# Performance work log

Measured on AMD Instinct MI355X. Metric: run time of the kernel, lower is better.

The kernel has to match this reference:

```python
import jax, jax.numpy as jnp
import numpy as np

TOKEN_NUMS = 206
IGNORE_IDX = -100
HALF_TOKEN = float((TOKEN_NUMS - 4) / 2)  # 101.0

B, S = 256, 682
T = 3 * S + 2  # 2048


def setup_inputs() -> dict:
    key = jax.random.key(0)
    k1, k2, k3, k4 = jax.random.split(key, 4)
    pred = jax.random.normal(k1, (B, T, TOKEN_NUMS), dtype=jnp.float32)
    gt_acc = jax.random.uniform(k2, (B, S), dtype=jnp.float32)
    gt_steer = jax.random.uniform(k3, (B, S), dtype=jnp.float32)
    gt_reverse = jax.random.randint(k4, (B, S), 0, 2, dtype=jnp.int64)
    return {"pred": pred, "gt_acc": gt_acc, "gt_steer": gt_steer, "gt_reverse": gt_reverse}


def _smooth_l1(pred, target):
    d = pred - target
    ad = jnp.abs(d)
    return jnp.mean(jnp.where(ad < 1.0, 0.5 * d * d, ad - 0.5))


def reference(pred, gt_acc, gt_steer, gt_reverse):
    pred_control = pred[:, :-2, :]
    acc_logits = pred_control[:, 0::3, :]    # [B, S, V]
    steer_logits = pred_control[:, 1::3, :]  # [B, S, V]
    rev_logits = pred_control[:, 2::3, :]    # [B, S, V]

    # softmax followed by argmax == argmax of logits (softmax is monotonic)
    acc_idx = jnp.argmax(acc_logits, axis=-1).reshape(-1).astype(jnp.float32)
    # vectorized detokenize_acc: if token > half: t/half - 1 else -(t/half - 1)
    pred_acc = jnp.where(acc_idx > HALF_TOKEN, acc_idx / HALF_TOKEN - 1.0,
                         1.0 - acc_idx / HALF_TOKEN)
    acc_val_loss = _smooth_l1(pred_acc, gt_acc.reshape(-1))

    steer_idx = jnp.argmax(steer_logits, axis=-1).reshape(-1).astype(jnp.float32)
    pred_steer = steer_idx / HALF_TOKEN - 1.0  # detokenize_steer
    steer_val_loss = _smooth_l1(pred_steer, gt_steer.reshape(-1))

    acc_steer_val_loss = acc_val_loss + steer_val_loss

    # reverse branch: sum softmax prob mass over the two token ranges per row
    rev_probs = jax.nn.softmax(rev_logits.reshape(-1, TOKEN_NUMS), axis=-1)
    p_no_reverse = jnp.sum(rev_probs[:, :101], axis=-1)
    p_reverse = jnp.sum(rev_probs[:, 101:], axis=-1)
    two_class = jnp.stack([p_no_reverse, p_reverse], axis=-1)  # [N, 2]
    # nn.CrossEntropyLoss applies log_softmax to its input (here: probabilities)
    logp = jax.nn.log_softmax(two_class, axis=-1)
    gt = gt_reverse.reshape(-1)
    valid = gt != IGNORE_IDX
    gt_safe = jnp.where(valid, gt, 0)
    nll = -jnp.take_along_axis(logp, gt_safe[:, None], axis=1)[:, 0]
    reverse_val_loss = jnp.sum(jnp.where(valid, nll, 0.0)) / jnp.maximum(
        jnp.sum(valid.astype(jnp.float32)), 1.0)

    return acc_steer_val_loss, reverse_val_loss
```

## Files before the change

kernel.cpp:

```cpp
#include <hip/hip_runtime.h>
#include <cstddef>

namespace {
constexpr int TOK   = 206;
constexpr int NROWS = 256 * 682;
constexpr int R     = 8;
constexpr int NBLK  = NROWS / R;
constexpr int LROW2 = 310;
constexpr int LDSF2 = R * LROW2 + 16;
constexpr int NSLOT = 64;
}

typedef float f32x4 __attribute__((ext_vector_type(4)));

__global__ __launch_bounds__(256) void cvl_main(
    const float* __restrict__ pred,
    const float* __restrict__ gt_acc,
    const float* __restrict__ gt_steer,
    const int*  __restrict__ gt_rev,
    double* __restrict__ ws)
{
    __shared__ alignas(16) double lds2[LDSF2];

    const int tid = threadIdx.x;
    const int r0  = blockIdx.x * R;

    const int sr = tid >> 5;
    const int sc = tid & 31;
    const int row = r0 + sr;
    const unsigned bb = (unsigned)row / 682u;
    const float* base = pred + (size_t)(3u * (unsigned)row + 2u * bb) * TOK;

    f32x4 v[5];
    #pragma unroll
    for (int k = 0; k < 4; ++k)
        v[k] = __builtin_nontemporal_load((const f32x4*)base + sc + 32 * k);
    const bool t5 = (sc < 26);
    f32x4 v4 = (f32x4){0.f, 0.f, 0.f, 0.f};
    if (t5) v4 = __builtin_nontemporal_load((const f32x4*)base + sc + 128);
    double tl = 0.0;
    if (sc == 31)
        tl = __builtin_nontemporal_load((const double*)(base + 616));
    const int   gt = gt_rev[row];
    const float ga = gt_acc[row];
    const float gs = gt_steer[row];

    f32x4* lrow4 = (f32x4*)(lds2 + sr * LROW2);
    #pragma unroll
    for (int k = 0; k < 4; ++k) lrow4[sc + 32 * k] = v[k];
    if (t5) lrow4[sc + 128] = v4;
    if (sc == 31) lds2[sr * LROW2 + 308] = tl;
    __syncthreads();

    const int lane = tid & 63;
    const int wid  = tid >> 6;
    const int l32  = lane & 31;
    const double* rp = &lds2[sr * LROW2];

    float2 q[10];
    #pragma unroll
    for (int k = 0; k < 10; ++k)
        q[k] = __builtin_bit_cast(float2, rp[l32 + 32 * k]);

    float aM = q[0].x; int aI = 2 * l32;
    if (q[0].y > aM) { aM = q[0].y; aI = 2 * l32 + 1; }
    #pragma unroll
    for (int k = 1; k <= 2; ++k) {
        const int t = 2 * (l32 + 32 * k);
        if (q[k].x > aM) { aM = q[k].x; aI = t; }
        if (q[k].y > aM) { aM = q[k].y; aI = t + 1; }
    }
    float sM = -INFINITY; int sI = 0;
    {
        const int i2 = l32 + 96;
        if (l32 < 7) {
            if (q[3].x > aM) { aM = q[3].x; aI = 2 * i2; }
            if (q[3].y > aM) { aM = q[3].y; aI = 2 * i2 + 1; }
        } else {
            sM = q[3].x; sI = 2 * i2 - 206;
            if (q[3].y > sM) { sM = q[3].y; sI = 2 * i2 - 205; }
        }
    }
    #pragma unroll
    for (int k = 4; k <= 5; ++k) {
        const int st = 2 * (l32 + 32 * k) - 206;
        if (q[k].x > sM) { sM = q[k].x; sI = st; }
        if (q[k].y > sM) { sM = q[k].y; sI = st + 1; }
    }
    float lo = 0.f, hi = 0.f;
    {
        if (l32 < 14) {
            const int st = 2 * (l32 + 192) - 206;
            if (q[6].x > sM) { sM = q[6].x; sI = st; }
            if (q[6].y > sM) { sM = q[6].y; sI = st + 1; }
        } else {
            lo += __expf(q[6].x) + __expf(q[6].y);
        }
    }
    lo += __expf(q[7].x) + __expf(q[7].y);
    {
        const float ex = __expf(q[8].x), ey = __expf(q[8].y);
        if (l32 == 0) lo += ex; else hi += ex;
        hi += ey;
    }
    if (l32 < 21) hi += __expf(q[9].x) + __expf(q[9].y);

    #pragma unroll
    for (int off = 16; off >= 1; off >>= 1) {
        const float av = __shfl_xor(aM, off);
        const int   ai = __shfl_xor(aI, off);
        if (av > aM) { aM = av; aI = ai; }
        const float sv = __shfl_xor(sM, off);
        const int   si = __shfl_xor(sI, off);
        if (sv > sM) { sM = sv; sI = si; }
        lo += __shfl_xor(lo, off);
        hi += __shfl_xor(hi, off);
    }

    float accS, steerS, revS = 0.f, cntS = 0.f;
    {
        const float Z    = lo + hi;
        const float pno  = lo / Z;
        const float prv  = hi / Z;
        const float ai_f = (float)aI;
        const float si_f = (float)sI;
        const float pa   = (ai_f > 101.f) ? (ai_f * (1.f / 101.f) - 1.f)
                                          : (1.f - ai_f * (1.f / 101.f));
        const float ps   = si_f * (1.f / 101.f) - 1.f;
        const float da   = pa - ga;
        const float dsv  = ps - gs;
        const float ada  = fabsf(da), ads = fabsf(dsv);
        accS   = (ada < 1.f) ? 0.5f * da * da   : ada - 0.5f;
        steerS = (ads < 1.f) ? 0.5f * dsv * dsv : ads - 0.5f;
        if (gt != -100) {
            const float m2 = fmaxf(pno, prv);
            revS = m2 + __logf(__expf(pno - m2) + __expf(prv - m2))
                   - ((gt == 0) ? pno : prv);
            cntS = 1.f;
        }
    }

    accS   += __shfl_xor(accS, 32);
    steerS += __shfl_xor(steerS, 32);
    revS   += __shfl_xor(revS, 32);
    cntS   += __shfl_xor(cntS, 32);

    __shared__ float red[4][4];
    if (lane == 0) {
        red[wid][0] = accS; red[wid][1] = steerS;
        red[wid][2] = revS; red[wid][3] = cntS;
    }
    __syncthreads();
    if (tid == 0) {
        double a = 0, st = 0, rr = 0, c = 0;
        for (int w = 0; w < 4; ++w) {
            a += red[w][0]; st += red[w][1]; rr += red[w][2]; c += red[w][3];
        }
        double* slot = ws + (size_t)(blockIdx.x & (NSLOT - 1)) * 4;
        atomicAdd(slot + 0, a);
        atomicAdd(slot + 1, st);
        atomicAdd(slot + 2, rr);
        atomicAdd(slot + 3, c);
    }
}

__global__ void cvl_init(double* __restrict__ ws) {
    const int i = blockIdx.x * blockDim.x + threadIdx.x;
    if (i < NSLOT * 4) ws[i] = 0.0;
}

__global__ void cvl_final(const double* __restrict__ ws, float* __restrict__ out) {
    const int t = threadIdx.x;
    double a = ws[4 * t], st = ws[4 * t + 1], r = ws[4 * t + 2], c = ws[4 * t + 3];
    #pragma unroll
    for (int off = 32; off >= 1; off >>= 1) {
        a  += __shfl_xor(a,  off);
        st += __shfl_xor(st, off);
        r  += __shfl_xor(r,  off);
        c  += __shfl_xor(c,  off);
    }
    if (t == 0) {
        const double n = (double)NROWS;
        out[0] = (float)(a / n + st / n);
        out[1] = (float)(r / fmax(c, 1.0));
    }
}

extern "C" void kernel_launch(void* const* d_in, const int* in_sizes, int n_in,
                              void* d_out, int out_size, void* d_ws, size_t ws_size,
                              hipStream_t stream) {
    const float* pred     = (const float*)d_in[0];
    const float* gt_acc   = (const float*)d_in[1];
    const float* gt_steer = (const float*)d_in[2];
    const int*   gt_rev   = (const int*)d_in[3];
    double* ws  = (double*)d_ws;
    float*  out = (float*)d_out;

    cvl_init<<<1, 256, 0, stream>>>(ws);
    cvl_main<<<NBLK, 256, 0, stream>>>(pred, gt_acc, gt_steer, gt_rev, ws);
    cvl_final<<<1, 64, 0, stream>>>(ws, out);
}
```

Baseline: 86.79 us.

## Use persistent grid-stride blocks with register prefetch of the next row group

The kernel moves from one block per 8-row group (21824 blocks) to a fixed grid of 2048 persistent blocks that loop over groups. Each block issues the global loads for its next group into registers right after the LDS barrier, so they overlap with the current group's argmax and softmax work. Partial sums now accumulate across iterations, which cuts the number of per-block atomics. The cost is higher register pressure from keeping the prefetch buffers live, which may lower occupancy and reduce the memory parallelism this bandwidth-bound kernel depends on.

```diff
diff --git a/kernel.cpp b/kernel.cpp
--- a/kernel.cpp
+++ b/kernel.cpp
@@ -5,7 +5,8 @@
 constexpr int TOK   = 206;
 constexpr int NROWS = 256 * 682;
 constexpr int R     = 8;
-constexpr int NBLK  = NROWS / R;
+constexpr int NGRP  = NROWS / R;
+constexpr int GRID  = 2048;
 constexpr int LROW2 = 310;
 constexpr int LDSF2 = R * LROW2 + 16;
 constexpr int NSLOT = 64;
@@ -23,121 +24,134 @@
     __shared__ alignas(16) double lds2[LDSF2];
 
     const int tid = threadIdx.x;
-    const int r0  = blockIdx.x * R;
-
-    const int sr = tid >> 5;
-    const int sc = tid & 31;
-    const int row = r0 + sr;
-    const unsigned bb = (unsigned)row / 682u;
-    const float* base = pred + (size_t)(3u * (unsigned)row + 2u * bb) * TOK;
-
-    f32x4 v[5];
-    #pragma unroll
-    for (int k = 0; k < 4; ++k)
-        v[k] = __builtin_nontemporal_load((const f32x4*)base + sc + 32 * k);
-    const bool t5 = (sc < 26);
-    f32x4 v4 = (f32x4){0.f, 0.f, 0.f, 0.f};
-    if (t5) v4 = __builtin_nontemporal_load((const f32x4*)base + sc + 128);
-    double tl = 0.0;
-    if (sc == 31)
-        tl = __builtin_nontemporal_load((const double*)(base + 616));
-    const int   gt = gt_rev[row];
-    const float ga = gt_acc[row];
-    const float gs = gt_steer[row];
-
-    f32x4* lrow4 = (f32x4*)(lds2 + sr * LROW2);
-    #pragma unroll
-    for (int k = 0; k < 4; ++k) lrow4[sc + 32 * k] = v[k];
-    if (t5) lrow4[sc + 128] = v4;
-    if (sc == 31) lds2[sr * LROW2 + 308] = tl;
-    __syncthreads();
-
+    const int sr  = tid >> 5;
+    const int sc  = tid & 31;
     const int lane = tid & 63;
     const int wid  = tid >> 6;
     const int l32  = lane & 31;
-    const double* rp = &lds2[sr * LROW2];
-
-    float2 q[10];
-    #pragma unroll
-    for (int k = 0; k < 10; ++k)
-        q[k] = __builtin_bit_cast(float2, rp[l32 + 32 * k]);
-
-    float aM = q[0].x; int aI = 2 * l32;
-    if (q[0].y > aM) { aM = q[0].y; aI = 2 * l32 + 1; }
-    #pragma unroll
-    for (int k = 1; k <= 2; ++k) {
-        const int t = 2 * (l32 + 32 * k);
-        if (q[k].x > aM) { aM = q[k].x; aI = t; }
-        if (q[k].y > aM) { aM = q[k].y; aI = t + 1; }
-    }
-    float sM = -INFINITY; int sI = 0;
-    {
-        const int i2 = l32 + 96;
-        if (l32 < 7) {
-            if (q[3].x > aM) { aM = q[3].x; aI = 2 * i2; }
-            if (q[3].y > aM) { aM = q[3].y; aI = 2 * i2 + 1; }
-        } else {
-            sM = q[3].x; sI = 2 * i2 - 206;
-            if (q[3].y > sM) { sM = q[3].y; sI = 2 * i2 - 205; }
-        }
-    }
-    #pragma unroll
-    for (int k = 4; k <= 5; ++k) {
-        const int st = 2 * (l32 + 32 * k) - 206;
-        if (q[k].x > sM) { sM = q[k].x; sI = st; }
-        if (q[k].y > sM) { sM = q[k].y; sI = st + 1; }
-    }
-    float lo = 0.f, hi = 0.f;
-    {
-        if (l32 < 14) {
-            const int st = 2 * (l32 + 192) - 206;
-            if (q[6].x > sM) { sM = q[6].x; sI = st; }
-            if (q[6].y > sM) { sM = q[6].y; sI = st + 1; }
-        } else {
-            lo += __expf(q[6].x) + __expf(q[6].y);
-        }
-    }
-    lo += __expf(q[7].x) + __expf(q[7].y);
-    {
-        const float ex = __expf(q[8].x), ey = __expf(q[8].y);
-        if (l32 == 0) lo += ex; else hi += ex;
-        hi += ey;
-    }
-    if (l32 < 21) hi += __expf(q[9].x) + __expf(q[9].y);
-
-    #pragma unroll
-    for (int off = 16; off >= 1; off >>= 1) {
-        const float av = __shfl_xor(aM, off);
-        const int   ai = __shfl_xor(aI, off);
-        if (av > aM) { aM = av; aI = ai; }
-        const float sv = __shfl_xor(sM, off);
-        const int   si = __shfl_xor(sI, off);
-        if (sv > sM) { sM = sv; sI = si; }
-        lo += __shfl_xor(lo, off);
-        hi += __shfl_xor(hi, off);
-    }
-
-    float accS, steerS, revS = 0.f, cntS = 0.f;
-    {
-        const float Z    = lo + hi;
-        const float pno  = lo / Z;
-        const float prv  = hi / Z;
-        const float ai_f = (float)aI;
-        const float si_f = (float)sI;
-        const float pa   = (ai_f > 101.f) ? (ai_f * (1.f / 101.f) - 1.f)
-                                          : (1.f - ai_f * (1.f / 101.f));
-        const float ps   = si_f * (1.f / 101.f) - 1.f;
-        const float da   = pa - ga;
-        const float dsv  = ps - gs;
-        const float ada  = fabsf(da), ads = fabsf(dsv);
-        accS   = (ada < 1.f) ? 0.5f * da * da   : ada - 0.5f;
-        steerS = (ads < 1.f) ? 0.5f * dsv * dsv : ads - 0.5f;
-        if (gt != -100) {
-            const float m2 = fmaxf(pno, prv);
-            revS = m2 + __logf(__expf(pno - m2) + __expf(prv - m2))
-                   - ((gt == 0) ? pno : prv);
-            cntS = 1.f;
-        }
+
+    float accS = 0.f, steerS = 0.f, revS = 0.f, cntS = 0.f;
+
+    f32x4 v[5];
+    double tl = 0.0;
+    int   gtN; float gaN, gsN;
+    auto load_group = [&](int g) {
+        const int row = g * R + sr;
+        const unsigned bb = (unsigned)row / 682u;
+        const float* base = pred + (size_t)(3u * (unsigned)row + 2u * bb) * TOK;
+        #pragma unroll
+        for (int k = 0; k < 4; ++k)
+            v[k] = __builtin_nontemporal_load((const f32x4*)base + sc + 32 * k);
+        if (sc < 26)
+            v[4] = __builtin_nontemporal_load((const f32x4*)base + sc + 128);
+        if (sc == 31)
+            tl = __builtin_nontemporal_load((const double*)(base + 616));
+        gtN = gt_rev[row];
+        gaN = gt_acc[row];
+        gsN = gt_steer[row];
+    };
+
+    int g = blockIdx.x;
+    if (g < NGRP) load_group(g);
+
+    while (g < NGRP) {
+        f32x4* lrow4 = (f32x4*)(lds2 + sr * LROW2);
+        #pragma unroll
+        for (int k = 0; k < 4; ++k) lrow4[sc + 32 * k] = v[k];
+        if (sc < 26) lrow4[sc + 128] = v[4];
+        if (sc == 31) lds2[sr * LROW2 + 308] = tl;
+        const int   gt = gtN;
+        const float ga = gaN;
+        const float gs = gsN;
+        __syncthreads();
+
+        const int gn = g + GRID;
+        if (gn < NGRP) load_group(gn);
+
+        const double* rp = &lds2[sr * LROW2];
+        float2 q[10];
+        #pragma unroll
+        for (int k = 0; k < 10; ++k)
+            q[k] = __builtin_bit_cast(float2, rp[l32 + 32 * k]);
+
+        float aM = q[0].x; int aI = 2 * l32;
+        if (q[0].y > aM) { aM = q[0].y; aI = 2 * l32 + 1; }
+        #pragma unroll
+        for (int k = 1; k <= 2; ++k) {
+            const int t = 2 * (l32 + 32 * k);
+            if (q[k].x > aM) { aM = q[k].x; aI = t; }
+            if (q[k].y > aM) { aM = q[k].y; aI = t + 1; }
+        }
+        float sM = -INFINITY; int sI = 0;
+        {
+            const int i2 = l32 + 96;
+            if (l32 < 7) {
+                if (q[3].x > aM) { aM = q[3].x; aI = 2 * i2; }
+                if (q[3].y > aM) { aM = q[3].y; aI = 2 * i2 + 1; }
+            } else {
+                sM = q[3].x; sI = 2 * i2 - 206;
+                if (q[3].y > sM) { sM = q[3].y; sI = 2 * i2 - 205; }
+            }
+        }
+        #pragma unroll
+        for (int k = 4; k <= 5; ++k) {
+            const int st = 2 * (l32 + 32 * k) - 206;
+            if (q[k].x > sM) { sM = q[k].x; sI = st; }
+            if (q[k].y > sM) { sM = q[k].y; sI = st + 1; }
+        }
+        float lo = 0.f, hi = 0.f;
+        {
+            if (l32 < 14) {
+                const int st = 2 * (l32 + 192) - 206;
+                if (q[6].x > sM) { sM = q[6].x; sI = st; }
+                if (q[6].y > sM) { sM = q[6].y; sI = st + 1; }
+            } else {
+                lo += __expf(q[6].x) + __expf(q[6].y);
+            }
+        }
+        lo += __expf(q[7].x) + __expf(q[7].y);
+        {
+            const float ex = __expf(q[8].x), ey = __expf(q[8].y);
+            if (l32 == 0) lo += ex; else hi += ex;
+            hi += ey;
+        }
+        if (l32 < 21) hi += __expf(q[9].x) + __expf(q[9].y);
+
+        #pragma unroll
+        for (int off = 16; off >= 1; off >>= 1) {
+            const float av = __shfl_xor(aM, off);
+            const int   ai = __shfl_xor(aI, off);
+            if (av > aM) { aM = av; aI = ai; }
+            const float sv = __shfl_xor(sM, off);
+            const int   si = __shfl_xor(sI, off);
+            if (sv > sM) { sM = sv; sI = si; }
+            lo += __shfl_xor(lo, off);
+            hi += __shfl_xor(hi, off);
+        }
+
+        {
+            const float Z    = lo + hi;
+            const float pno  = lo / Z;
+            const float prv  = hi / Z;
+            const float ai_f = (float)aI;
+            const float si_f = (float)sI;
+            const float pa   = (ai_f > 101.f) ? (ai_f * (1.f / 101.f) - 1.f)
+                                              : (1.f - ai_f * (1.f / 101.f));
+            const float ps   = si_f * (1.f / 101.f) - 1.f;
+            const float da   = pa - ga;
+            const float dsv  = ps - gs;
+            const float ada  = fabsf(da), ads = fabsf(dsv);
+            accS   += (ada < 1.f) ? 0.5f * da * da   : ada - 0.5f;
+            steerS += (ads < 1.f) ? 0.5f * dsv * dsv : ads - 0.5f;
+            if (gt != -100) {
+                const float m2 = fmaxf(pno, prv);
+                revS += m2 + __logf(__expf(pno - m2) + __expf(prv - m2))
+                        - ((gt == 0) ? pno : prv);
+                cntS += 1.f;
+            }
+        }
+        __syncthreads();
+        g = gn;
     }
 
     accS   += __shfl_xor(accS, 32);
@@ -197,6 +211,6 @@
     float*  out = (float*)d_out;
 
     cvl_init<<<1, 256, 0, stream>>>(ws);
-    cvl_main<<<NBLK, 256, 0, stream>>>(pred, gt_acc, gt_steer, gt_rev, ws);
+    cvl_main<<<GRID, 256, 0, stream>>>(pred, gt_acc, gt_steer, gt_rev, ws);
     cvl_final<<<1, 64, 0, stream>>>(ws, out);
 }
```

New measurement: 82.37 us. 1.05x faster.
